# Optimization experiments

Measured on AMD Instinct MI355X. Metric: run time of the kernel, lower is better.

## Reference

```python
import jax, jax.numpy as jnp
import numpy as np

MIN_DISTANCE = 1.0
CONSTRAINT_WEIGHT = 0.02


def setup_inputs() -> dict:
    key = jax.random.key(0)
    pos = jax.random.normal(key, (16384, 3), dtype=jnp.float32) * 5.0
    return {"pos": pos}


def reference(pos):
    # pos: [N, 3]
    n = pos.shape[0]
    # Pairwise Euclidean distances via the gram trick (avoids [N,N,3] diff tensor)
    sq = jnp.sum(pos * pos, axis=-1)                      # [N]
    d2 = sq[:, None] + sq[None, :] - 2.0 * (pos @ pos.T)  # [N, N]
    d2 = jnp.maximum(d2, 0.0)
    eye = jnp.eye(n, dtype=bool)
    # keep sqrt away from 0 on the diagonal (masked to inf anyway)
    dist = jnp.sqrt(jnp.where(eye, 1.0, d2))
    dist = jnp.where(eye, jnp.inf, dist)                  # masked_fill(eye, inf)
    violations = jnp.maximum(MIN_DISTANCE - dist, 0.0)    # clamp(min=0)
    constraint_loss = jnp.mean(violations) * CONSTRAINT_WEIGHT
    return pos, constraint_loss
```

## Files before the change

kernel.cpp:

```cpp
#include <hip/hip_runtime.h>


constexpr int   N     = 16384;
constexpr int   BLOCK = 256;
constexpr int   GSZ   = 512;
constexpr int   IPT   = GSZ / BLOCK;
constexpr int   NG    = N / GSZ;
constexpr int   F     = 8;
constexpr int   NB    = NG * F;
constexpr int   QB    = 4;
constexpr int   NBINS = 256;
constexpr float BINW_INV = 4.0f;
constexpr int   MARGIN = 5;
constexpr int   CH    = 288;
constexpr int   NHB   = N / BLOCK;

__device__ __forceinline__ int zcell(float z) {
    int c = (int)floorf(z * BINW_INV) + NBINS / 2;
    return min(max(c, 0), NBINS - 1);
}

__global__ void __launch_bounds__(BLOCK)
prep_kernel(const float* __restrict__ pos, float* __restrict__ out,
            unsigned int* __restrict__ histPart, unsigned int* __restrict__ crk,
            float* __restrict__ acc, unsigned int* __restrict__ cnt) {
    __shared__ unsigned int lh[NBINS];
    const int b = blockIdx.x, t = threadIdx.x;
    const int gt = b * BLOCK + t;
    lh[t] = 0u;
    if (gt == 0) { *acc = 0.0f; *cnt = 0u; }
    __syncthreads();
    if (gt < (N * 3) / 4) {
        reinterpret_cast<float4*>(out)[gt] = reinterpret_cast<const float4*>(pos)[gt];
    }
    const float z = pos[3 * gt + 2];
    const int cell = zcell(z);
    const unsigned int rank = atomicAdd(&lh[cell], 1u);
    crk[gt] = (unsigned int)cell | (rank << 16);
    __syncthreads();
    histPart[b * NBINS + t] = lh[t];
}

__global__ void __launch_bounds__(BLOCK)
scatter_kernel(const float* __restrict__ pos, const unsigned int* __restrict__ histPart,
               const unsigned int* __restrict__ crk, float4* __restrict__ jt4s,
               int* __restrict__ jendArr) {
    __shared__ int sm[NBINS];
    __shared__ int beforeB[NBINS];
    const int b = blockIdx.x, t = threadIdx.x;
    int v = 0, bef = 0;
    #pragma unroll 8
    for (int p = 0; p < NHB; ++p) {
        const int hv = (int)histPart[p * NBINS + t];
        if (p == b) bef = v;
        v += hv;
    }
    sm[t] = v; beforeB[t] = bef;
    __syncthreads();
    for (int off = 1; off < NBINS; off <<= 1) {
        const int a = (t >= off) ? sm[t - off] : 0;
        __syncthreads();
        sm[t] += a;
        __syncthreads();
    }
    const int gt = b * BLOCK + t;
    const unsigned int cr = crk[gt];
    const int cell = (int)(cr & 0xffffu);
    const int rank = (int)(cr >> 16);
    const int ex   = (cell > 0) ? sm[cell - 1] : 0;
    const int dst  = ex + beforeB[cell] + rank;
    const float x = pos[3 * gt], y = pos[3 * gt + 1], z = pos[3 * gt + 2];
    jt4s[dst] = make_float4(x, y, z, fmaf(x, x, fmaf(y, y, z * z)));
    if (b == 0 && t < NG) {
        const int p = (t + 1) * GSZ - 1;
        int lo = 0, hi = NBINS - 1;
        while (lo < hi) {
            const int mid = (lo + hi) >> 1;
            if (sm[mid] >= p + 1) hi = mid; else lo = mid + 1;
        }
        const int jidx = lo + MARGIN;
        jendArr[t] = (jidx >= NBINS) ? N : sm[jidx - 1];
    }
}

template <bool MASKED>
__device__ __forceinline__ float cols(const float4* __restrict__ jsm,
                                      int clen, int jbase, int i0,
                                      const float (&xi2)[IPT], const float (&yi2)[IPT],
                                      const float (&zi2)[IPT], const float (&sqi)[IPT]) {
    float s = 0.0f;
    for (int c = 0; c < clen; c += QB) {
        #pragma unroll
        for (int u = 0; u < QB; ++u) {
            const float4 pj = jsm[c + u];
            const int jq = jbase + c + u;
            #pragma unroll
            for (int k = 0; k < IPT; ++k) {
                float d = fmaf(xi2[k], pj.x, pj.w);
                d = fmaf(yi2[k], pj.y, d);
                d = fmaf(zi2[k], pj.z, d);
                const float d2 = fmaxf(d + sqi[k], 0.0f);
                float w = 1.0f - __builtin_amdgcn_sqrtf(d2);
                w = fmaxf(w, 0.0f);
                if (MASKED) w = (jq > i0 + k * BLOCK) ? w : 0.0f;
                s += w;
            }
        }
    }
    return s;
}

__global__ void __launch_bounds__(BLOCK)
pair_kernel(const float4* __restrict__ jt4s, const int* __restrict__ jendArr,
            float* __restrict__ out, float* __restrict__ acc,
            unsigned int* __restrict__ cnt) {
    __shared__ float4 jsm[CH + QB];
    __shared__ float wsum[BLOCK / 64];
    const int b = blockIdx.x;
    const int t = threadIdx.x;
    const int g = b >> 3, f = b & (F - 1);
    const int gstart = g * GSZ;
    const int i0 = gstart + t;

    const float4 w0 = jt4s[i0];
    const float4 w1 = jt4s[i0 + BLOCK];

    const int jend = jendArr[g];
    const int jbeg = gstart + 1;
    const int jlen = jend - jbeg;
    const int seg  = (((jlen + F - 1) / F) + QB - 1) & ~(QB - 1);
    const int j0   = jbeg + f * seg;
    const int len  = min(seg, jend - j0);

    float xi2[IPT], yi2[IPT], zi2[IPT], sqi[IPT];
    xi2[0] = -2.0f * w0.x; yi2[0] = -2.0f * w0.y; zi2[0] = -2.0f * w0.z; sqi[0] = w0.w;
    xi2[1] = -2.0f * w1.x; yi2[1] = -2.0f * w1.y; zi2[1] = -2.0f * w1.z; sqi[1] = w1.w;

    float s = 0.0f;
    for (int cs = 0; cs < len; cs += CH) {
        const int clen = min(CH, len - cs);
        if (t < clen)         jsm[t]         = jt4s[j0 + cs + t];
        if (t + BLOCK < clen) jsm[t + BLOCK] = jt4s[j0 + cs + t + BLOCK];
        if (t < QB) jsm[clen + t] = make_float4(0.0f, 0.0f, 1.0e6f, 4.0e12f);
        __syncthreads();
        if (j0 + cs < gstart + GSZ)
            s += cols<true >(jsm, clen, j0 + cs, i0, xi2, yi2, zi2, sqi);
        else
            s += cols<false>(jsm, clen, j0 + cs, i0, xi2, yi2, zi2, sqi);
        __syncthreads();
    }

    for (int off = 32; off > 0; off >>= 1) s += __shfl_down(s, off);
    if ((t & 63) == 0) wsum[t >> 6] = s;
    __syncthreads();
    if (t == 0) {
        float bs = 0.0f;
        #pragma unroll
        for (int w = 0; w < BLOCK / 64; ++w) bs += wsum[w];
        atomicAdd(acc, bs);
        __threadfence();
        const unsigned int done = atomicAdd(cnt, 1u);
        if (done == (unsigned int)(NB - 1)) {
            __threadfence();
            const float total = atomicAdd(acc, 0.0f);
            const double mean = 2.0 * (double)total / ((double)N * (double)N);
            out[(size_t)N * 3] = (float)(mean * 0.02);
        }
    }
}

extern "C" void kernel_launch(void* const* d_in, const int* in_sizes, int n_in,
                              void* d_out, int out_size, void* d_ws, size_t ws_size,
                              hipStream_t stream) {
    const float* pos = (const float*)d_in[0];
    float* out = (float*)d_out;
    float*        acc      = (float*)d_ws;
    unsigned int* cnt      = (unsigned int*)d_ws + 1;
    int*          jendArr  = (int*)((char*)d_ws + 256);
    unsigned int* histPart = (unsigned int*)((char*)d_ws + 4096);
    unsigned int* crk      = (unsigned int*)((char*)d_ws + 69632);
    float4*       jt4s     = (float4*)((char*)d_ws + 135168);

    prep_kernel   <<<NHB, BLOCK, 0, stream>>>(pos, out, histPart, crk, acc, cnt);
    scatter_kernel<<<NHB, BLOCK, 0, stream>>>(pos, histPart, crk, jt4s, jendArr);
    pair_kernel   <<<NB,  BLOCK, 0, stream>>>(jt4s, jendArr, out, acc, cnt);
}
```

Measured before the change: 78.90 us.

## Fuse scatter into pair kernel by gathering sorted tiles directly per block

Removes the separate scatter kernel and its global sorted array. Each pair block now recomputes the bin prefix sums itself and walks all points' cell/rank codes, so it can pick out its i-tile and j-chunk straight into shared memory. The j-chunk size grows to 384. This saves one launch and a global round trip, but every block redundantly scans all histograms and all N codes for every chunk, and it uses much more shared memory, which may lower occupancy.

```diff
diff --git a/kernel.cpp b/kernel.cpp
--- a/kernel.cpp
+++ b/kernel.cpp
@@ -12,7 +12,7 @@
 constexpr int   NBINS = 256;
 constexpr float BINW_INV = 4.0f;
 constexpr int   MARGIN = 5;
-constexpr int   CH    = 288;
+constexpr int   CH2   = 384;
 constexpr int   NHB   = N / BLOCK;
 
 __device__ __forceinline__ int zcell(float z) {
@@ -23,6 +23,7 @@
 __global__ void __launch_bounds__(BLOCK)
 prep_kernel(const float* __restrict__ pos, float* __restrict__ out,
             unsigned int* __restrict__ histPart, unsigned int* __restrict__ crk,
+            float4* __restrict__ p4,
             float* __restrict__ acc, unsigned int* __restrict__ cnt) {
     __shared__ unsigned int lh[NBINS];
     const int b = blockIdx.x, t = threadIdx.x;
@@ -33,54 +34,13 @@
     if (gt < (N * 3) / 4) {
         reinterpret_cast<float4*>(out)[gt] = reinterpret_cast<const float4*>(pos)[gt];
     }
-    const float z = pos[3 * gt + 2];
+    const float x = pos[3 * gt], y = pos[3 * gt + 1], z = pos[3 * gt + 2];
+    p4[gt] = make_float4(x, y, z, fmaf(x, x, fmaf(y, y, z * z)));
     const int cell = zcell(z);
     const unsigned int rank = atomicAdd(&lh[cell], 1u);
     crk[gt] = (unsigned int)cell | (rank << 16);
     __syncthreads();
     histPart[b * NBINS + t] = lh[t];
-}
-
-__global__ void __launch_bounds__(BLOCK)
-scatter_kernel(const float* __restrict__ pos, const unsigned int* __restrict__ histPart,
-               const unsigned int* __restrict__ crk, float4* __restrict__ jt4s,
-               int* __restrict__ jendArr) {
-    __shared__ int sm[NBINS];
-    __shared__ int beforeB[NBINS];
-    const int b = blockIdx.x, t = threadIdx.x;
-    int v = 0, bef = 0;
-    #pragma unroll 8
-    for (int p = 0; p < NHB; ++p) {
-        const int hv = (int)histPart[p * NBINS + t];
-        if (p == b) bef = v;
-        v += hv;
-    }
-    sm[t] = v; beforeB[t] = bef;
-    __syncthreads();
-    for (int off = 1; off < NBINS; off <<= 1) {
-        const int a = (t >= off) ? sm[t - off] : 0;
-        __syncthreads();
-        sm[t] += a;
-        __syncthreads();
-    }
-    const int gt = b * BLOCK + t;
-    const unsigned int cr = crk[gt];
-    const int cell = (int)(cr & 0xffffu);
-    const int rank = (int)(cr >> 16);
-    const int ex   = (cell > 0) ? sm[cell - 1] : 0;
-    const int dst  = ex + beforeB[cell] + rank;
-    const float x = pos[3 * gt], y = pos[3 * gt + 1], z = pos[3 * gt + 2];
-    jt4s[dst] = make_float4(x, y, z, fmaf(x, x, fmaf(y, y, z * z)));
-    if (b == 0 && t < NG) {
-        const int p = (t + 1) * GSZ - 1;
-        int lo = 0, hi = NBINS - 1;
-        while (lo < hi) {
-            const int mid = (lo + hi) >> 1;
-            if (sm[mid] >= p + 1) hi = mid; else lo = mid + 1;
-        }
-        const int jidx = lo + MARGIN;
-        jendArr[t] = (jidx >= NBINS) ? N : sm[jidx - 1];
-    }
 }
 
 template <bool MASKED>
@@ -111,42 +71,86 @@
 }
 
 __global__ void __launch_bounds__(BLOCK)
-pair_kernel(const float4* __restrict__ jt4s, const int* __restrict__ jendArr,
-            float* __restrict__ out, float* __restrict__ acc,
-            unsigned int* __restrict__ cnt) {
-    __shared__ float4 jsm[CH + QB];
+fused_kernel(const unsigned int* __restrict__ histPart,
+             const unsigned int* __restrict__ crk, const float4* __restrict__ p4,
+             float* __restrict__ out, float* __restrict__ acc,
+             unsigned int* __restrict__ cnt) {
+    __shared__ unsigned short prefT[NHB][NBINS];
+    __shared__ int sm[NBINS];
+    __shared__ float4 ism[GSZ];
+    __shared__ float4 jsm[CH2 + QB];
     __shared__ float wsum[BLOCK / 64];
-    const int b = blockIdx.x;
-    const int t = threadIdx.x;
+    const int b = blockIdx.x, t = threadIdx.x;
     const int g = b >> 3, f = b & (F - 1);
     const int gstart = g * GSZ;
-    const int i0 = gstart + t;
 
-    const float4 w0 = jt4s[i0];
-    const float4 w1 = jt4s[i0 + BLOCK];
+    int run = 0;
+    for (int p = 0; p < NHB; ++p) {
+        prefT[p][t] = (unsigned short)run;
+        run += (int)histPart[p * NBINS + t];
+    }
+    sm[t] = run;
+    __syncthreads();
+    for (int off = 1; off < NBINS; off <<= 1) {
+        const int a = (t >= off) ? sm[t - off] : 0;
+        __syncthreads();
+        sm[t] += a;
+        __syncthreads();
+    }
 
-    const int jend = jendArr[g];
+    int jend;
+    {
+        const int target = gstart + GSZ;
+        int lo = 0, hi = NBINS - 1;
+        while (lo < hi) {
+            const int mid = (lo + hi) >> 1;
+            if (sm[mid] >= target) hi = mid; else lo = mid + 1;
+        }
+        const int jidx = lo + MARGIN;
+        jend = (jidx >= NBINS) ? N : sm[jidx - 1];
+    }
     const int jbeg = gstart + 1;
     const int jlen = jend - jbeg;
     const int seg  = (((jlen + F - 1) / F) + QB - 1) & ~(QB - 1);
     const int j0   = jbeg + f * seg;
     const int len  = min(seg, jend - j0);
-
-    float xi2[IPT], yi2[IPT], zi2[IPT], sqi[IPT];
-    xi2[0] = -2.0f * w0.x; yi2[0] = -2.0f * w0.y; zi2[0] = -2.0f * w0.z; sqi[0] = w0.w;
-    xi2[1] = -2.0f * w1.x; yi2[1] = -2.0f * w1.y; zi2[1] = -2.0f * w1.z; sqi[1] = w1.w;
+    const int i0   = gstart + t;
 
     float s = 0.0f;
-    for (int cs = 0; cs < len; cs += CH) {
-        const int clen = min(CH, len - cs);
-        if (t < clen)         jsm[t]         = jt4s[j0 + cs + t];
-        if (t + BLOCK < clen) jsm[t + BLOCK] = jt4s[j0 + cs + t + BLOCK];
+    float xi2[IPT] = {0.f, 0.f}, yi2[IPT] = {0.f, 0.f};
+    float zi2[IPT] = {0.f, 0.f}, sqi[IPT] = {0.f, 0.f};
+
+    for (int cs = 0; cs < len; cs += CH2) {
+        const int j0c  = j0 + cs;
+        const int clen = min(CH2, len - cs);
+        for (int p = 0; p < NHB; ++p) {
+            const unsigned int cr = crk[p * BLOCK + t];
+            const int cell = (int)(cr & 0xffffu);
+            const int rank = (int)(cr >> 16);
+            const int ex   = (cell > 0) ? sm[cell - 1] : 0;
+            const int gdst = ex + (int)prefT[p][cell] + rank;
+            const unsigned int ui = (unsigned int)(gdst - gstart);
+            const unsigned int uj = (unsigned int)(gdst - j0c);
+            const bool ini = (cs == 0) && (ui < (unsigned int)GSZ);
+            const bool inj = (uj < (unsigned int)clen);
+            if (ini || inj) {
+                const float4 v = p4[p * BLOCK + t];
+                if (ini) ism[ui] = v;
+                if (inj) jsm[uj] = v;
+            }
+        }
         if (t < QB) jsm[clen + t] = make_float4(0.0f, 0.0f, 1.0e6f, 4.0e12f);
         __syncthreads();
-        if (j0 + cs < gstart + GSZ)
-            s += cols<true >(jsm, clen, j0 + cs, i0, xi2, yi2, zi2, sqi);
+        if (cs == 0) {
+            const float4 w0 = ism[t];
+            const float4 w1 = ism[t + BLOCK];
+            xi2[0] = -2.0f*w0.x; yi2[0] = -2.0f*w0.y; zi2[0] = -2.0f*w0.z; sqi[0] = w0.w;
+            xi2[1] = -2.0f*w1.x; yi2[1] = -2.0f*w1.y; zi2[1] = -2.0f*w1.z; sqi[1] = w1.w;
+        }
+        if (j0c < gstart + GSZ)
+            s += cols<true >(jsm, clen, j0c, i0, xi2, yi2, zi2, sqi);
         else
-            s += cols<false>(jsm, clen, j0 + cs, i0, xi2, yi2, zi2, sqi);
+            s += cols<false>(jsm, clen, j0c, i0, xi2, yi2, zi2, sqi);
         __syncthreads();
     }
 
@@ -176,12 +180,10 @@
     float* out = (float*)d_out;
     float*        acc      = (float*)d_ws;
     unsigned int* cnt      = (unsigned int*)d_ws + 1;
-    int*          jendArr  = (int*)((char*)d_ws + 256);
     unsigned int* histPart = (unsigned int*)((char*)d_ws + 4096);
     unsigned int* crk      = (unsigned int*)((char*)d_ws + 69632);
-    float4*       jt4s     = (float4*)((char*)d_ws + 135168);
+    float4*       p4       = (float4*)((char*)d_ws + 135168);
 
-    prep_kernel   <<<NHB, BLOCK, 0, stream>>>(pos, out, histPart, crk, acc, cnt);
-    scatter_kernel<<<NHB, BLOCK, 0, stream>>>(pos, histPart, crk, jt4s, jendArr);
-    pair_kernel   <<<NB,  BLOCK, 0, stream>>>(jt4s, jendArr, out, acc, cnt);
+    prep_kernel <<<NHB, BLOCK, 0, stream>>>(pos, out, histPart, crk, p4, acc, cnt);
+    fused_kernel<<<NB,  BLOCK, 0, stream>>>(histPart, crk, p4, out, acc, cnt);
 }
```

Result: slower. 101.1 us (+28.1%).

## Use one i-point per thread with 512-thread pair blocks

Applied to the files above, without the earlier changes.

The pair kernel drops per-thread register blocking of two i-points and instead launches 512-thread blocks, each thread handling one i-point. The shared j chunk grows to 384 entries and is loaded with a single pass. This raises the number of waves per CU to hide sqrt and LDS latency. In exchange, each LDS j load is reused by only one i-point instead of two.

```diff
diff --git a/kernel.cpp b/kernel.cpp
--- a/kernel.cpp
+++ b/kernel.cpp
@@ -3,8 +3,9 @@
 
 constexpr int   N     = 16384;
 constexpr int   BLOCK = 256;
+constexpr int   PBLK  = 512;
 constexpr int   GSZ   = 512;
-constexpr int   IPT   = GSZ / BLOCK;
+constexpr int   IPT   = 1;
 constexpr int   NG    = N / GSZ;
 constexpr int   F     = 8;
 constexpr int   NB    = NG * F;
@@ -12,7 +13,7 @@
 constexpr int   NBINS = 256;
 constexpr float BINW_INV = 4.0f;
 constexpr int   MARGIN = 5;
-constexpr int   CH    = 288;
+constexpr int   CH    = 384;
 constexpr int   NHB   = N / BLOCK;
 
 __device__ __forceinline__ int zcell(float z) {
@@ -86,36 +87,32 @@
 template <bool MASKED>
 __device__ __forceinline__ float cols(const float4* __restrict__ jsm,
                                       int clen, int jbase, int i0,
-                                      const float (&xi2)[IPT], const float (&yi2)[IPT],
-                                      const float (&zi2)[IPT], const float (&sqi)[IPT]) {
+                                      float xi2, float yi2, float zi2, float sqi) {
     float s = 0.0f;
     for (int c = 0; c < clen; c += QB) {
         #pragma unroll
         for (int u = 0; u < QB; ++u) {
             const float4 pj = jsm[c + u];
             const int jq = jbase + c + u;
-            #pragma unroll
-            for (int k = 0; k < IPT; ++k) {
-                float d = fmaf(xi2[k], pj.x, pj.w);
-                d = fmaf(yi2[k], pj.y, d);
-                d = fmaf(zi2[k], pj.z, d);
-                const float d2 = fmaxf(d + sqi[k], 0.0f);
-                float w = 1.0f - __builtin_amdgcn_sqrtf(d2);
-                w = fmaxf(w, 0.0f);
-                if (MASKED) w = (jq > i0 + k * BLOCK) ? w : 0.0f;
-                s += w;
-            }
+            float d = fmaf(xi2, pj.x, pj.w);
+            d = fmaf(yi2, pj.y, d);
+            d = fmaf(zi2, pj.z, d);
+            const float d2 = fmaxf(d + sqi, 0.0f);
+            float w = 1.0f - __builtin_amdgcn_sqrtf(d2);
+            w = fmaxf(w, 0.0f);
+            if (MASKED) w = (jq > i0) ? w : 0.0f;
+            s += w;
         }
     }
     return s;
 }
 
-__global__ void __launch_bounds__(BLOCK)
+__global__ void __launch_bounds__(PBLK)
 pair_kernel(const float4* __restrict__ jt4s, const int* __restrict__ jendArr,
             float* __restrict__ out, float* __restrict__ acc,
             unsigned int* __restrict__ cnt) {
     __shared__ float4 jsm[CH + QB];
-    __shared__ float wsum[BLOCK / 64];
+    __shared__ float wsum[PBLK / 64];
     const int b = blockIdx.x;
     const int t = threadIdx.x;
     const int g = b >> 3, f = b & (F - 1);
@@ -123,7 +120,6 @@
     const int i0 = gstart + t;
 
     const float4 w0 = jt4s[i0];
-    const float4 w1 = jt4s[i0 + BLOCK];
 
     const int jend = jendArr[g];
     const int jbeg = gstart + 1;
@@ -132,16 +128,14 @@
     const int j0   = jbeg + f * seg;
     const int len  = min(seg, jend - j0);
 
-    float xi2[IPT], yi2[IPT], zi2[IPT], sqi[IPT];
-    xi2[0] = -2.0f * w0.x; yi2[0] = -2.0f * w0.y; zi2[0] = -2.0f * w0.z; sqi[0] = w0.w;
-    xi2[1] = -2.0f * w1.x; yi2[1] = -2.0f * w1.y; zi2[1] = -2.0f * w1.z; sqi[1] = w1.w;
+    const float xi2 = -2.0f * w0.x, yi2 = -2.0f * w0.y, zi2 = -2.0f * w0.z;
+    const float sqi = w0.w;
 
     float s = 0.0f;
     for (int cs = 0; cs < len; cs += CH) {
         const int clen = min(CH, len - cs);
-        if (t < clen)         jsm[t]         = jt4s[j0 + cs + t];
-        if (t + BLOCK < clen) jsm[t + BLOCK] = jt4s[j0 + cs + t + BLOCK];
-        if (t < QB) jsm[clen + t] = make_float4(0.0f, 0.0f, 1.0e6f, 4.0e12f);
+        if (t < clen) jsm[t] = jt4s[j0 + cs + t];
+        if (t < QB)   jsm[clen + t] = make_float4(0.0f, 0.0f, 1.0e6f, 4.0e12f);
         __syncthreads();
         if (j0 + cs < gstart + GSZ)
             s += cols<true >(jsm, clen, j0 + cs, i0, xi2, yi2, zi2, sqi);
@@ -156,7 +150,7 @@
     if (t == 0) {
         float bs = 0.0f;
         #pragma unroll
-        for (int w = 0; w < BLOCK / 64; ++w) bs += wsum[w];
+        for (int w = 0; w < PBLK / 64; ++w) bs += wsum[w];
         atomicAdd(acc, bs);
         __threadfence();
         const unsigned int done = atomicAdd(cnt, 1u);
@@ -183,5 +177,5 @@
 
     prep_kernel   <<<NHB, BLOCK, 0, stream>>>(pos, out, histPart, crk, acc, cnt);
     scatter_kernel<<<NHB, BLOCK, 0, stream>>>(pos, histPart, crk, jt4s, jendArr);
-    pair_kernel   <<<NB,  BLOCK, 0, stream>>>(jt4s, jendArr, out, acc, cnt);
+    pair_kernel   <<<NB,  PBLK,  0, stream>>>(jt4s, jendArr, out, acc, cnt);
 }
```

After: 75.75 us (median of 2 runs). 1.04x faster.
